# Performance work log

Hardware: AMD Instinct MI355X
Metric: run time of the kernel (lower is better)

The kernel has to match this reference:

```python
import jax, jax.numpy as jnp
import numpy as np

B, C, N = 32, 1024, 256   # N=256 is hard-coded by query/key Conv1d in_channels
DQ = 256 // 4             # 64
EPS = 1e-5                # BatchNorm eps


def setup_inputs() -> dict:
    key = jax.random.key(0)
    ks = jax.random.split(key, 16)
    def bn_params(k, ch):
        k1, k2, k3, k4 = jax.random.split(k, 4)
        return (jax.random.uniform(k1, (ch,), jnp.float32, 0.5, 1.5),   # gamma
                jax.random.normal(k2, (ch,), jnp.float32) * 0.1,        # beta
                jax.random.normal(k3, (ch,), jnp.float32) * 0.1,        # running mean
                jax.random.uniform(k4, (ch,), jnp.float32, 0.5, 1.5))   # running var
    bn1 = bn_params(ks[4], DQ)
    bn2 = bn_params(ks[5], DQ)
    bn3 = bn_params(ks[6], C)
    return {
        "x": jax.random.normal(ks[0], (B, C, N), jnp.float32),
        "Wq": jax.random.normal(ks[1], (DQ, N), jnp.float32) * (1.0 / np.sqrt(N)),
        "Wk": jax.random.normal(ks[2], (DQ, N), jnp.float32) * (1.0 / np.sqrt(N)),
        "Wv": jax.random.normal(ks[3], (C, C), jnp.float32) * (1.0 / np.sqrt(C)),
        "bn1_g": bn1[0], "bn1_b": bn1[1], "bn1_m": bn1[2], "bn1_v": bn1[3],
        "bn2_g": bn2[0], "bn2_b": bn2[1], "bn2_m": bn2[2], "bn2_v": bn2[3],
        "bn3_g": bn3[0], "bn3_b": bn3[1], "bn3_m": bn3[2], "bn3_v": bn3[3],
        "alpha": jnp.full((1,), 0.1, jnp.float32),  # torch init is 0; 0.1 keeps the branch active
    }


def _bn(y, g, b, m, v):
    # eval-mode BatchNorm1d over channel axis 1 of (B, ch, L)
    scale = g / jnp.sqrt(v + EPS)
    return (y - m[None, :, None]) * scale[None, :, None] + b[None, :, None]


def reference(x, Wq, Wk, Wv,
              bn1_g, bn1_b, bn1_m, bn1_v,
              bn2_g, bn2_b, bn2_m, bn2_v,
              bn3_g, bn3_b, bn3_m, bn3_v,
              alpha):
    x_hat = jnp.swapaxes(x, 1, 2)                                   # (B, N, C)
    q = jax.nn.relu(_bn(jnp.einsum('on,bnc->boc', Wq, x_hat), bn1_g, bn1_b, bn1_m, bn1_v))  # (B, DQ, C)
    k = jax.nn.relu(_bn(jnp.einsum('on,bnc->boc', Wk, x_hat), bn2_g, bn2_b, bn2_m, bn2_v))  # (B, DQ, C)
    sim = jnp.einsum('bkc,bkd->bcd', k, q)                          # (B, C, C) channel affinity
    aff = jax.nn.softmax(jnp.max(sim, axis=-1, keepdims=True) - sim, axis=-1)
    v = jax.nn.relu(_bn(jnp.einsum('oc,bcn->bon', Wv, x), bn3_g, bn3_b, bn3_m, bn3_v))      # (B, C, N)
    out = jnp.einsum('bcd,bdn->bcn', aff, v)                        # (B, C, N)
    return alpha * out + x
```

## Files before the change

kernel.cpp:

```cpp
#include <hip/hip_runtime.h>
#include <hip/hip_bf16.h>

#define B_  32
#define C_  1024
#define N_  256
#define DQ_ 64

typedef __bf16 bf16_t;
typedef __bf16 bf16x8 __attribute__((ext_vector_type(8)));
typedef float  f32x4  __attribute__((ext_vector_type(4)));

static __device__ __forceinline__ f32x4 mfma16(bf16x8 a, bf16x8 b, f32x4 c) {
  return __builtin_amdgcn_mfma_f32_16x16x32_bf16(a, b, c, 0, 0, 0);
}

static __device__ __forceinline__ bf16x8 ldcvt(const float* p) {
  const float4 a = *(const float4*)p;
  const float4 b = *(const float4*)(p + 4);
  bf16x8 r;
  r[0] = (bf16_t)a.x; r[1] = (bf16_t)a.y; r[2] = (bf16_t)a.z; r[3] = (bf16_t)a.w;
  r[4] = (bf16_t)b.x; r[5] = (bf16_t)b.y; r[6] = (bf16_t)b.z; r[7] = (bf16_t)b.w;
  return r;
}

#define WAIT_VMCNT(N) __builtin_amdgcn_s_waitcnt(0x0F70 | (N))

__global__ __launch_bounds__(256) void k_trans(const float* __restrict__ x,
                                               bf16_t* __restrict__ xT) {
  __shared__ bf16_t tile[32][34];
  const int b  = blockIdx.z;
  const int n0 = blockIdx.x * 32, c0 = blockIdx.y * 32;
  const int tx = threadIdx.x, ty = threadIdx.y;
  const float* xb = x + (size_t)b * C_ * N_;
  bf16_t*     xtb = xT + (size_t)b * N_ * C_;
#pragma unroll
  for (int i = 0; i < 4; ++i)
    tile[ty + i * 8][tx] = (bf16_t)xb[(size_t)(c0 + ty + i * 8) * N_ + (n0 + tx)];
  __syncthreads();
#pragma unroll
  for (int i = 0; i < 4; ++i)
    xtb[(size_t)(n0 + ty + i * 8) * C_ + (c0 + tx)] = tile[tx][ty + i * 8];
}

__global__ __launch_bounds__(256) void k_cvt(const float* __restrict__ Wv,
                                             const float* __restrict__ Wq,
                                             const float* __restrict__ Wk,
                                             bf16_t* __restrict__ Wvb,
                                             bf16_t* __restrict__ Wqkb) {
  const int gid = blockIdx.x * 256 + threadIdx.x;
  if (blockIdx.x < 512) {
    const int i = gid * 8;
    *(bf16x8*)(Wvb + i) = ldcvt(Wv + i);
  } else {
    const int g2 = (gid - 512 * 256) * 8;
    if (g2 < 16384) *(bf16x8*)(Wqkb + g2) = ldcvt(Wq + g2);
    else            *(bf16x8*)(Wqkb + g2) = ldcvt(Wk + (g2 - 16384));
  }
}

__global__ __launch_bounds__(256) void k_qk(const float* __restrict__ x,
                                            const bf16_t* __restrict__ Wqkb,
                                            const float* __restrict__ g1,
                                            const float* __restrict__ b1,
                                            const float* __restrict__ m1,
                                            const float* __restrict__ v1,
                                            const float* __restrict__ g2,
                                            const float* __restrict__ b2,
                                            const float* __restrict__ m2,
                                            const float* __restrict__ v2,
                                            bf16_t* __restrict__ qt,
                                            bf16_t* __restrict__ kt) {
  __shared__ __align__(16) bf16_t Ws[128 * 256];
  const int tid  = threadIdx.x;
  const int wave = tid >> 6;
  const int lane = tid & 63;
  const int quad = lane >> 4;
  const int l16  = lane & 15;
  const int b    = blockIdx.y;
  const int c16  = blockIdx.x * 64 + wave * 16;
  const float* xb = x + (size_t)b * C_ * N_;

#pragma unroll
  for (int t = 0; t < 16; ++t) {
    const int o = wave * 32 + t * 2 + (lane >> 5);
    const int s = lane & 31;
    const int g = (s - o) & 31;
    const bf16_t* src = Wqkb + (size_t)o * N_ + g * 8;
    __builtin_amdgcn_global_load_lds(
        (const __attribute__((address_space(1))) void*)src,
        (__attribute__((address_space(3))) void*)(Ws + (wave * 32 + t * 2) * N_ + lane * 8),
        16, 0, 0);
  }

  bf16x8 bx[8];
#pragma unroll
  for (int ks = 0; ks < 8; ++ks)
    bx[ks] = ldcvt(xb + (size_t)(c16 + l16) * N_ + ks * 32 + quad * 8);

  __syncthreads();

  f32x4 acc[8];
#pragma unroll
  for (int i = 0; i < 8; ++i) acc[i] = (f32x4){0.f, 0.f, 0.f, 0.f};

#pragma unroll
  for (int ks = 0; ks < 8; ++ks) {
    const int ch = ks * 4 + quad;
#pragma unroll
    for (int i = 0; i < 8; ++i) {
      const int orow = i * 16 + l16;
      const int s = (ch + orow) & 31;
      const bf16x8 aw = *(const bf16x8*)(Ws + (size_t)orow * N_ + s * 8);
      acc[i] = mfma16(aw, bx[ks], acc[i]);
    }
  }

#pragma unroll
  for (int i = 0; i < 8; ++i) {
    const bool isq = (i < 4);
    bf16_t* dst = isq ? qt : kt;
#pragma unroll
    for (int r = 0; r < 4; ++r) {
      const int o = (i & 3) * 16 + quad * 4 + r;
      const float sc = (isq ? g1[o] : g2[o]) * rsqrtf((isq ? v1[o] : v2[o]) + 1e-5f);
      const float mm = isq ? m1[o] : m2[o];
      const float bt = isq ? b1[o] : b2[o];
      const int c = c16 + l16;
      float y = (acc[i][r] - mm) * sc + bt;
      y = fmaxf(y, 0.f);
      dst[((size_t)b * C_ + c) * DQ_ + o] = (bf16_t)y;
    }
  }
}

static __device__ __forceinline__ void stage32(const bf16_t* grow0, size_t gstride,
                                               bf16_t* tile, int wave, int lane) {
#pragma unroll
  for (int t = 0; t < 4; ++t) {
    const int rb = wave * 32 + t * 8;
    const int r  = rb + (lane >> 3);
    const int g  = ((lane & 7) - r) & 7;
    const bf16_t* src = grow0 + (size_t)r * gstride + g * 8;
    __builtin_amdgcn_global_load_lds(
        (const __attribute__((address_space(1))) void*)src,
        (__attribute__((address_space(3))) void*)(tile + rb * 64), 16, 0, 0);
  }
}

__global__ __launch_bounds__(256, 2) void k_vgemm(const bf16_t* __restrict__ Wvb,
                                                  const bf16_t* __restrict__ xT,
                                                  const float* __restrict__ g,
                                                  const float* __restrict__ be,
                                                  const float* __restrict__ mu,
                                                  const float* __restrict__ va,
                                                  bf16_t* __restrict__ vT) {
  __shared__ __align__(16) bf16_t As[2][128 * 64];
  __shared__ __align__(16) bf16_t Bs[2][128 * 64];
  const int tid  = threadIdx.x;
  const int wave = tid >> 6;
  const int lane = tid & 63;
  const int quad = lane >> 4;
  const int l16  = lane & 15;
  const int o0 = blockIdx.x * 128;
  const int r0 = blockIdx.y * 128;
  const bf16_t* Ab = Wvb + (size_t)o0 * C_;
  const bf16_t* Bb = xT + (size_t)r0 * C_;
  const int wr = (wave >> 1) * 64, wc = (wave & 1) * 64;

  stage32(Ab, C_, (bf16_t*)As[0], wave, lane);
  stage32(Bb, C_, (bf16_t*)Bs[0], wave, lane);

  f32x4 acc[4][4];
#pragma unroll
  for (int i = 0; i < 4; ++i)
#pragma unroll
    for (int j = 0; j < 4; ++j) acc[i][j] = (f32x4){0.f, 0.f, 0.f, 0.f};

  for (int ks = 0; ks < 16; ++ks) {
    __syncthreads();
    const bf16_t* ca = As[ks & 1];
    const bf16_t* cb = Bs[ks & 1];
    if (ks < 15) {
      stage32(Ab + (ks + 1) * 64, C_, (bf16_t*)As[(ks + 1) & 1], wave, lane);
      stage32(Bb + (ks + 1) * 64, C_, (bf16_t*)Bs[(ks + 1) & 1], wave, lane);
    }
#pragma unroll
    for (int ksub = 0; ksub < 2; ++ksub) {
      bf16x8 a[4], bfr[4];
#pragma unroll
      for (int i = 0; i < 4; ++i) {
        const int r = wr + i * 16 + l16;
        const int s = ((ksub * 4 + quad) + r) & 7;
        a[i] = *(const bf16x8*)(ca + r * 64 + s * 8);
      }
#pragma unroll
      for (int j = 0; j < 4; ++j) {
        const int r = wc + j * 16 + l16;
        const int s = ((ksub * 4 + quad) + r) & 7;
        bfr[j] = *(const bf16x8*)(cb + r * 64 + s * 8);
      }
#pragma unroll
      for (int i = 0; i < 4; ++i)
#pragma unroll
        for (int j = 0; j < 4; ++j)
          acc[i][j] = mfma16(a[i], bfr[j], acc[i][j]);
    }
  }

#pragma unroll
  for (int i = 0; i < 4; ++i)
#pragma unroll
    for (int r = 0; r < 4; ++r) {
      const int o = o0 + wr + i * 16 + quad * 4 + r;
      const float sc = g[o] * rsqrtf(va[o] + 1e-5f);
      const float mm = mu[o], bt = be[o];
#pragma unroll
      for (int j = 0; j < 4; ++j) {
        const int rG = r0 + wc + j * 16 + l16;
        float y = (acc[i][j][r] - mm) * sc + bt;
        y = fmaxf(y, 0.f);
        vT[(size_t)rG * C_ + o] = (bf16_t)y;
      }
    }
}

static __device__ __forceinline__ int eaddr16(int c, int d) {
  const int ch = d >> 3;
  const int ph = (ch & ~7) | ((ch + c) & 7);
  return (c << 10) + (ph << 3) + (d & 7);
}

__global__ __launch_bounds__(256, 2) void k_fused(const bf16_t* __restrict__ qt,
                                                  const bf16_t* __restrict__ kt,
                                                  const bf16_t* __restrict__ vT,
                                                  const float* __restrict__ x,
                                                  const float* __restrict__ alphap,
                                                  float* __restrict__ out) {
  __shared__ __align__(16) bf16_t ebuf[16 * 1024];
  __shared__ __align__(16) bf16_t vs[2][4][64 * 32];
  __shared__ float redmin[4][16];
  __shared__ float redsum[4][16];
  __shared__ float rowmin[16];
  __shared__ float rowrinv[16];

  const int tid  = threadIdx.x;
  const int wave = tid >> 6;
  const int lane = tid & 63;
  const int quad = lane >> 4;
  const int l16  = lane & 15;
  const int id   = blockIdx.x;
  const int b    = ((id & 7) << 2) | (id >> 9);
  const int c0   = ((id >> 3) & 63) << 4;
  const int dbase = wave * 256;

  const bf16_t* ktb = kt + ((size_t)b * C_ + c0) * DQ_;
  const bf16_t* qb  = qt + (size_t)b * C_ * DQ_;
  bf16x8 am[2];
  am[0] = *(const bf16x8*)(ktb + (size_t)l16 * DQ_ + quad * 8);
  am[1] = *(const bf16x8*)(ktb + (size_t)l16 * DQ_ + 32 + quad * 8);
  f32x4 sim[16];
#pragma unroll
  for (int nt = 0; nt < 16; ++nt) {
    const bf16_t* qrow = qb + (size_t)(dbase + nt * 16 + l16) * DQ_ + quad * 8;
    const bf16x8 b0 = *(const bf16x8*)(qrow);
    const bf16x8 b1 = *(const bf16x8*)(qrow + 32);
    f32x4 acc = (f32x4){0.f, 0.f, 0.f, 0.f};
    acc = mfma16(am[0], b0, acc);
    acc = mfma16(am[1], b1, acc);
    sim[nt] = acc;
  }

  const bf16_t* vb = vT + ((size_t)b * N_ + wave * 64) * C_;
  bf16_t* myvs[2] = {(bf16_t*)vs[0][wave], (bf16_t*)vs[1][wave]};
#pragma unroll
  for (int t = 0; t < 4; ++t) {
    const int r = t * 16 + (lane >> 2);
    const int gg = ((lane & 3) - (r + (r >> 2))) & 3;
    const bf16_t* src = vb + (size_t)r * C_ + gg * 8;
    __builtin_amdgcn_global_load_lds(
        (const __attribute__((address_space(1))) void*)src,
        (__attribute__((address_space(3))) void*)(myvs[0] + t * 512 + lane * 8),
        16, 0, 0);
  }

  float pmin[4];
#pragma unroll
  for (int r = 0; r < 4; ++r) pmin[r] = sim[0][r];
#pragma unroll
  for (int nt = 1; nt < 16; ++nt)
#pragma unroll
    for (int r = 0; r < 4; ++r) pmin[r] = fminf(pmin[r], sim[nt][r]);
#pragma unroll
  for (int m = 1; m < 16; m <<= 1)
#pragma unroll
    for (int r = 0; r < 4; ++r) pmin[r] = fminf(pmin[r], __shfl_xor(pmin[r], m));
  if (l16 == 0)
#pragma unroll
    for (int r = 0; r < 4; ++r) redmin[wave][quad * 4 + r] = pmin[r];
  __syncthreads();
  if (tid < 16)
    rowmin[tid] = fminf(fminf(redmin[0][tid], redmin[1][tid]),
                        fminf(redmin[2][tid], redmin[3][tid]));
  __syncthreads();

  float mn[4], psum[4] = {0.f, 0.f, 0.f, 0.f};
#pragma unroll
  for (int r = 0; r < 4; ++r) mn[r] = rowmin[quad * 4 + r];
#pragma unroll
  for (int nt = 0; nt < 16; ++nt) {
    const int d = dbase + nt * 16 + l16;
#pragma unroll
    for (int r = 0; r < 4; ++r) {
      const int c = quad * 4 + r;
      const float e = __expf(mn[r] - sim[nt][r]);
      ebuf[eaddr16(c, d)] = (bf16_t)e;
      psum[r] += e;
    }
  }
#pragma unroll
  for (int m = 1; m < 16; m <<= 1)
#pragma unroll
    for (int r = 0; r < 4; ++r) psum[r] += __shfl_xor(psum[r], m);
  if (l16 == 0)
#pragma unroll
    for (int r = 0; r < 4; ++r) redsum[wave][quad * 4 + r] = psum[r];
  __syncthreads();
  if (tid < 16)
    rowrinv[tid] = 1.f / (redsum[0][tid] + redsum[1][tid] + redsum[2][tid] + redsum[3][tid]);
  __syncthreads();

  f32x4 oacc[4];
#pragma unroll
  for (int jn = 0; jn < 4; ++jn) oacc[jn] = (f32x4){0.f, 0.f, 0.f, 0.f};

  for (int ks = 0; ks < 32; ++ks) {
    const bf16_t* cur = myvs[ks & 1];
    if (ks < 31) {
      bf16_t* nxt = myvs[(ks + 1) & 1];
      const int koff = (ks + 1) * 32;
#pragma unroll
      for (int t = 0; t < 4; ++t) {
        const int r = t * 16 + (lane >> 2);
        const int gg = ((lane & 3) - (r + (r >> 2))) & 3;
        const bf16_t* src = vb + (size_t)r * C_ + koff + gg * 8;
        __builtin_amdgcn_global_load_lds(
            (const __attribute__((address_space(1))) void*)src,
            (__attribute__((address_space(3))) void*)(nxt + t * 512 + lane * 8),
            16, 0, 0);
      }
      WAIT_VMCNT(4);
    } else {
      WAIT_VMCNT(0);
    }
    const int gch = ks * 4 + quad;
    const int ph  = (gch & ~7) | ((gch + l16) & 7);
    const bf16x8 ae = *(const bf16x8*)(ebuf + ((size_t)l16 << 10) + ph * 8);
    bf16x8 bv[4];
#pragma unroll
    for (int jn = 0; jn < 4; ++jn) {
      const int rl = jn * 16 + l16;
      const int s = (quad + rl + (rl >> 2)) & 3;
      bv[jn] = *(const bf16x8*)(cur + rl * 32 + s * 8);
    }
#pragma unroll
    for (int jn = 0; jn < 4; ++jn)
      oacc[jn] = mfma16(ae, bv[jn], oacc[jn]);
  }

  const float alpha = alphap[0];
#pragma unroll
  for (int jn = 0; jn < 4; ++jn)
#pragma unroll
    for (int r = 0; r < 4; ++r) {
      const int c = c0 + quad * 4 + r;
      const int n = wave * 64 + jn * 16 + l16;
      const size_t idx = ((size_t)b * C_ + c) * N_ + n;
      out[idx] = alpha * (oacc[jn][r] * rowrinv[quad * 4 + r]) + x[idx];
    }
}

extern "C" void kernel_launch(void* const* d_in, const int* in_sizes, int n_in,
                              void* d_out, int out_size, void* d_ws, size_t ws_size,
                              hipStream_t stream) {
  const float* x    = (const float*)d_in[0];
  const float* Wq   = (const float*)d_in[1];
  const float* Wk   = (const float*)d_in[2];
  const float* Wv   = (const float*)d_in[3];
  const float* bn1g = (const float*)d_in[4];
  const float* bn1b = (const float*)d_in[5];
  const float* bn1m = (const float*)d_in[6];
  const float* bn1v = (const float*)d_in[7];
  const float* bn2g = (const float*)d_in[8];
  const float* bn2b = (const float*)d_in[9];
  const float* bn2m = (const float*)d_in[10];
  const float* bn2v = (const float*)d_in[11];
  const float* bn3g = (const float*)d_in[12];
  const float* bn3b = (const float*)d_in[13];
  const float* bn3m = (const float*)d_in[14];
  const float* bn3v = (const float*)d_in[15];
  const float* alph = (const float*)d_in[16];
  float* outp = (float*)d_out;

  char* ws = (char*)d_ws;
  bf16_t* qt   = (bf16_t*)(ws);
  bf16_t* kt   = (bf16_t*)(ws + (size_t)(4u << 20));
  bf16_t* vT   = (bf16_t*)(ws + (size_t)(8u << 20));
  bf16_t* xT   = (bf16_t*)(ws + (size_t)(24u << 20));
  bf16_t* Wvb  = (bf16_t*)(ws + (size_t)(40u << 20));
  bf16_t* Wqkb = (bf16_t*)(ws + (size_t)(42u << 20));

  k_trans<<<dim3(8, 32, 32), dim3(32, 8, 1), 0, stream>>>(x, xT);
  k_cvt<<<dim3(528), 256, 0, stream>>>(Wv, Wq, Wk, Wvb, Wqkb);
  k_qk<<<dim3(16, 32), 256, 0, stream>>>(x, Wqkb,
                                         bn1g, bn1b, bn1m, bn1v,
                                         bn2g, bn2b, bn2m, bn2v, qt, kt);
  k_vgemm<<<dim3(8, 64), 256, 0, stream>>>(Wvb, xT, bn3g, bn3b, bn3m, bn3v, vT);
  k_fused<<<dim3(2048), 256, 0, stream>>>(qt, kt, vT, x, alph, outp);
}
```

Before: 256.7 us.

## Restructure fused attention kernel: 32-row tiles, register softmax, split-K LDS reduction

Each block of the fused kernel now covers 32 channel rows instead of 16, which halves the grid. Each wave takes a 256-wide slice of the d dimension. The exp-softmax values stay in registers and are rearranged into MFMA A-fragments with cross-lane shuffles, so the LDS ebuf staging and the double-buffered async V loads are gone. Each wave then reads V directly from global memory over its own d slice and reduces partial outputs into a shared fp32 accumulator with LDS atomics before the final epilogue. The aim is to reuse V loads across 32 rows and remove LDS staging, at the cost of LDS atomic contention, unpipelined global loads, and a large shared buffer that may limit occupancy.

```diff
diff --git a/kernel.cpp b/kernel.cpp
--- a/kernel.cpp
+++ b/kernel.cpp
@@ -8,6 +8,7 @@
 
 typedef __bf16 bf16_t;
 typedef __bf16 bf16x8 __attribute__((ext_vector_type(8)));
+typedef __bf16 bf16x4 __attribute__((ext_vector_type(4)));
 typedef float  f32x4  __attribute__((ext_vector_type(4)));
 
 static __device__ __forceinline__ f32x4 mfma16(bf16x8 a, bf16x8 b, f32x4 c) {
@@ -22,8 +23,6 @@
   r[4] = (bf16_t)b.x; r[5] = (bf16_t)b.y; r[6] = (bf16_t)b.z; r[7] = (bf16_t)b.w;
   return r;
 }
-
-#define WAIT_VMCNT(N) __builtin_amdgcn_s_waitcnt(0x0F70 | (N))
 
 __global__ __launch_bounds__(256) void k_trans(const float* __restrict__ x,
                                                bf16_t* __restrict__ xT) {
@@ -224,24 +223,17 @@
     }
 }
 
-static __device__ __forceinline__ int eaddr16(int c, int d) {
-  const int ch = d >> 3;
-  const int ph = (ch & ~7) | ((ch + c) & 7);
-  return (c << 10) + (ph << 3) + (d & 7);
-}
-
 __global__ __launch_bounds__(256, 2) void k_fused(const bf16_t* __restrict__ qt,
                                                   const bf16_t* __restrict__ kt,
                                                   const bf16_t* __restrict__ vT,
                                                   const float* __restrict__ x,
                                                   const float* __restrict__ alphap,
                                                   float* __restrict__ out) {
-  __shared__ __align__(16) bf16_t ebuf[16 * 1024];
-  __shared__ __align__(16) bf16_t vs[2][4][64 * 32];
-  __shared__ float redmin[4][16];
-  __shared__ float redsum[4][16];
-  __shared__ float rowmin[16];
-  __shared__ float rowrinv[16];
+  __shared__ float outacc[32][257];
+  __shared__ float redmin[4][32];
+  __shared__ float redsum[4][32];
+  __shared__ float rowmin[32];
+  __shared__ float rowrinv[32];
 
   const int tid  = threadIdx.x;
   const int wave = tid >> 6;
@@ -249,134 +241,149 @@
   const int quad = lane >> 4;
   const int l16  = lane & 15;
   const int id   = blockIdx.x;
-  const int b    = ((id & 7) << 2) | (id >> 9);
-  const int c0   = ((id >> 3) & 63) << 4;
-  const int dbase = wave * 256;
-
+  const int b    = ((id & 7) << 2) | (id >> 8);
+  const int c0   = ((id >> 3) & 31) << 5;
+  const int d0   = wave * 256;
+
+  {
+    float* fl = &outacc[0][0];
+    for (int i = tid; i < 32 * 257; i += 256) fl[i] = 0.f;
+  }
+
+  const bf16_t* qb  = qt + (size_t)b * C_ * DQ_;
   const bf16_t* ktb = kt + ((size_t)b * C_ + c0) * DQ_;
-  const bf16_t* qb  = qt + (size_t)b * C_ * DQ_;
-  bf16x8 am[2];
-  am[0] = *(const bf16x8*)(ktb + (size_t)l16 * DQ_ + quad * 8);
-  am[1] = *(const bf16x8*)(ktb + (size_t)l16 * DQ_ + 32 + quad * 8);
-  f32x4 sim[16];
-#pragma unroll
-  for (int nt = 0; nt < 16; ++nt) {
-    const bf16_t* qrow = qb + (size_t)(dbase + nt * 16 + l16) * DQ_ + quad * 8;
-    const bf16x8 b0 = *(const bf16x8*)(qrow);
-    const bf16x8 b1 = *(const bf16x8*)(qrow + 32);
-    f32x4 acc = (f32x4){0.f, 0.f, 0.f, 0.f};
-    acc = mfma16(am[0], b0, acc);
-    acc = mfma16(am[1], b1, acc);
-    sim[nt] = acc;
-  }
-
-  const bf16_t* vb = vT + ((size_t)b * N_ + wave * 64) * C_;
-  bf16_t* myvs[2] = {(bf16_t*)vs[0][wave], (bf16_t*)vs[1][wave]};
-#pragma unroll
-  for (int t = 0; t < 4; ++t) {
-    const int r = t * 16 + (lane >> 2);
-    const int gg = ((lane & 3) - (r + (r >> 2))) & 3;
-    const bf16_t* src = vb + (size_t)r * C_ + gg * 8;
-    __builtin_amdgcn_global_load_lds(
-        (const __attribute__((address_space(1))) void*)src,
-        (__attribute__((address_space(3))) void*)(myvs[0] + t * 512 + lane * 8),
-        16, 0, 0);
-  }
-
-  float pmin[4];
-#pragma unroll
-  for (int r = 0; r < 4; ++r) pmin[r] = sim[0][r];
-#pragma unroll
-  for (int nt = 1; nt < 16; ++nt)
-#pragma unroll
-    for (int r = 0; r < 4; ++r) pmin[r] = fminf(pmin[r], sim[nt][r]);
-#pragma unroll
-  for (int m = 1; m < 16; m <<= 1)
-#pragma unroll
-    for (int r = 0; r < 4; ++r) pmin[r] = fminf(pmin[r], __shfl_xor(pmin[r], m));
-  if (l16 == 0)
-#pragma unroll
-    for (int r = 0; r < 4; ++r) redmin[wave][quad * 4 + r] = pmin[r];
-  __syncthreads();
-  if (tid < 16)
+  bf16x8 kf[2][2];
+#pragma unroll
+  for (int ci = 0; ci < 2; ++ci)
+#pragma unroll
+    for (int ks = 0; ks < 2; ++ks)
+      kf[ci][ks] = *(const bf16x8*)(ktb + (size_t)(ci * 16 + l16) * DQ_ + ks * 32 + quad * 8);
+
+  f32x4 sim[2][16];
+#pragma unroll
+  for (int ci = 0; ci < 2; ++ci)
+#pragma unroll
+    for (int dt = 0; dt < 16; ++dt) sim[ci][dt] = (f32x4){0.f, 0.f, 0.f, 0.f};
+
+#pragma unroll
+  for (int dt = 0; dt < 16; ++dt) {
+    const bf16_t* qrow = qb + (size_t)(d0 + dt * 16 + l16) * DQ_;
+    const bf16x8 q0 = *(const bf16x8*)(qrow + quad * 8);
+    const bf16x8 q1 = *(const bf16x8*)(qrow + 32 + quad * 8);
+#pragma unroll
+    for (int ci = 0; ci < 2; ++ci) {
+      sim[ci][dt] = mfma16(q0, kf[ci][0], sim[ci][dt]);
+      sim[ci][dt] = mfma16(q1, kf[ci][1], sim[ci][dt]);
+    }
+  }
+
+  float pmin[2];
+#pragma unroll
+  for (int ci = 0; ci < 2; ++ci) {
+    float m = sim[ci][0][0];
+#pragma unroll
+    for (int dt = 0; dt < 16; ++dt)
+#pragma unroll
+      for (int r = 0; r < 4; ++r) m = fminf(m, sim[ci][dt][r]);
+    m = fminf(m, __shfl_xor(m, 16));
+    m = fminf(m, __shfl_xor(m, 32));
+    pmin[ci] = m;
+  }
+  if (lane < 16) {
+    redmin[wave][l16]      = pmin[0];
+    redmin[wave][16 + l16] = pmin[1];
+  }
+  __syncthreads();
+  if (tid < 32)
     rowmin[tid] = fminf(fminf(redmin[0][tid], redmin[1][tid]),
                         fminf(redmin[2][tid], redmin[3][tid]));
   __syncthreads();
 
-  float mn[4], psum[4] = {0.f, 0.f, 0.f, 0.f};
-#pragma unroll
-  for (int r = 0; r < 4; ++r) mn[r] = rowmin[quad * 4 + r];
-#pragma unroll
-  for (int nt = 0; nt < 16; ++nt) {
-    const int d = dbase + nt * 16 + l16;
-#pragma unroll
-    for (int r = 0; r < 4; ++r) {
-      const int c = quad * 4 + r;
-      const float e = __expf(mn[r] - sim[nt][r]);
-      ebuf[eaddr16(c, d)] = (bf16_t)e;
-      psum[r] += e;
-    }
-  }
-#pragma unroll
-  for (int m = 1; m < 16; m <<= 1)
-#pragma unroll
-    for (int r = 0; r < 4; ++r) psum[r] += __shfl_xor(psum[r], m);
-  if (l16 == 0)
-#pragma unroll
-    for (int r = 0; r < 4; ++r) redsum[wave][quad * 4 + r] = psum[r];
-  __syncthreads();
-  if (tid < 16)
+  union U2 { bf16x4 v; uint2 u; };
+  U2 E[2][16];
+  float psum[2];
+#pragma unroll
+  for (int ci = 0; ci < 2; ++ci) {
+    const float mn = rowmin[ci * 16 + l16];
+    float s = 0.f;
+#pragma unroll
+    for (int dt = 0; dt < 16; ++dt) {
+      bf16x4 ev;
+#pragma unroll
+      for (int r = 0; r < 4; ++r) {
+        const float e = __expf(mn - sim[ci][dt][r]);
+        ev[r] = (bf16_t)e;
+        s += e;
+      }
+      E[ci][dt].v = ev;
+    }
+    s += __shfl_xor(s, 16);
+    s += __shfl_xor(s, 32);
+    psum[ci] = s;
+  }
+  if (lane < 16) {
+    redsum[wave][l16]      = psum[0];
+    redsum[wave][16 + l16] = psum[1];
+  }
+  __syncthreads();
+  if (tid < 32)
     rowrinv[tid] = 1.f / (redsum[0][tid] + redsum[1][tid] + redsum[2][tid] + redsum[3][tid]);
   __syncthreads();
 
-  f32x4 oacc[4];
-#pragma unroll
-  for (int jn = 0; jn < 4; ++jn) oacc[jn] = (f32x4){0.f, 0.f, 0.f, 0.f};
-
-  for (int ks = 0; ks < 32; ++ks) {
-    const bf16_t* cur = myvs[ks & 1];
-    if (ks < 31) {
-      bf16_t* nxt = myvs[(ks + 1) & 1];
-      const int koff = (ks + 1) * 32;
-#pragma unroll
-      for (int t = 0; t < 4; ++t) {
-        const int r = t * 16 + (lane >> 2);
-        const int gg = ((lane & 3) - (r + (r >> 2))) & 3;
-        const bf16_t* src = vb + (size_t)r * C_ + koff + gg * 8;
-        __builtin_amdgcn_global_load_lds(
-            (const __attribute__((address_space(1))) void*)src,
-            (__attribute__((address_space(3))) void*)(nxt + t * 512 + lane * 8),
-            16, 0, 0);
-      }
-      WAIT_VMCNT(4);
-    } else {
-      WAIT_VMCNT(0);
-    }
-    const int gch = ks * 4 + quad;
-    const int ph  = (gch & ~7) | ((gch + l16) & 7);
-    const bf16x8 ae = *(const bf16x8*)(ebuf + ((size_t)l16 << 10) + ph * 8);
-    bf16x8 bv[4];
-#pragma unroll
-    for (int jn = 0; jn < 4; ++jn) {
-      const int rl = jn * 16 + l16;
-      const int s = (quad + rl + (rl >> 2)) & 3;
-      bv[jn] = *(const bf16x8*)(cur + rl * 32 + s * 8);
-    }
-#pragma unroll
-    for (int jn = 0; jn < 4; ++jn)
-      oacc[jn] = mfma16(ae, bv[jn], oacc[jn]);
-  }
+  const int src0 = ((quad & 1) << 5) + l16;
+  const int src1 = src0 + 16;
+  const bool hiTile = (quad >> 1) & 1;
+  union U4 { bf16x8 v; uint4 u; };
+  U4 afrag[2][8];
+#pragma unroll
+  for (int ci = 0; ci < 2; ++ci)
+#pragma unroll
+    for (int p = 0; p < 8; ++p) {
+      uint2 e0 = E[ci][2 * p].u, e1 = E[ci][2 * p + 1].u;
+      const unsigned a0x = __shfl((int)e0.x, src0), a0y = __shfl((int)e0.y, src0);
+      const unsigned b0x = __shfl((int)e1.x, src0), b0y = __shfl((int)e1.y, src0);
+      const unsigned a1x = __shfl((int)e0.x, src1), a1y = __shfl((int)e0.y, src1);
+      const unsigned b1x = __shfl((int)e1.x, src1), b1y = __shfl((int)e1.y, src1);
+      U4 f;
+      f.u.x = hiTile ? b0x : a0x;
+      f.u.y = hiTile ? b0y : a0y;
+      f.u.z = hiTile ? b1x : a1x;
+      f.u.w = hiTile ? b1y : a1y;
+      afrag[ci][p] = f;
+    }
+
+  const bf16_t* vb = vT + (size_t)b * N_ * C_ + d0;
+#pragma unroll 2
+  for (int jn = 0; jn < 16; ++jn) {
+    const bf16_t* vrow = vb + (size_t)(jn * 16 + l16) * C_;
+    bf16x8 bfr[8];
+#pragma unroll
+    for (int p = 0; p < 8; ++p)
+      bfr[p] = *(const bf16x8*)(vrow + p * 32 + quad * 8);
+    f32x4 oacc[2];
+    oacc[0] = (f32x4){0.f, 0.f, 0.f, 0.f};
+    oacc[1] = (f32x4){0.f, 0.f, 0.f, 0.f};
+#pragma unroll
+    for (int p = 0; p < 8; ++p) {
+      oacc[0] = mfma16(afrag[0][p].v, bfr[p], oacc[0]);
+      oacc[1] = mfma16(afrag[1][p].v, bfr[p], oacc[1]);
+    }
+    const int n = jn * 16 + l16;
+#pragma unroll
+    for (int ci = 0; ci < 2; ++ci)
+#pragma unroll
+      for (int r = 0; r < 4; ++r)
+        atomicAdd(&outacc[ci * 16 + quad * 4 + r][n], oacc[ci][r]);
+  }
+  __syncthreads();
 
   const float alpha = alphap[0];
-#pragma unroll
-  for (int jn = 0; jn < 4; ++jn)
-#pragma unroll
-    for (int r = 0; r < 4; ++r) {
-      const int c = c0 + quad * 4 + r;
-      const int n = wave * 64 + jn * 16 + l16;
-      const size_t idx = ((size_t)b * C_ + c) * N_ + n;
-      out[idx] = alpha * (oacc[jn][r] * rowrinv[quad * 4 + r]) + x[idx];
-    }
+  const int n = tid;
+  const float* xrow = x + ((size_t)b * C_ + c0) * N_ + n;
+  float* orow = out + ((size_t)b * C_ + c0) * N_ + n;
+#pragma unroll
+  for (int c = 0; c < 32; ++c)
+    orow[c * N_] = alpha * (outacc[c][n] * rowrinv[c]) + xrow[c * N_];
 }
 
 extern "C" void kernel_launch(void* const* d_in, const int* in_sizes, int n_in,
@@ -415,5 +422,5 @@
                                          bn1g, bn1b, bn1m, bn1v,
                                          bn2g, bn2b, bn2m, bn2v, qt, kt);
   k_vgemm<<<dim3(8, 64), 256, 0, stream>>>(Wvb, xT, bn3g, bn3b, bn3m, bn3v, vT);
-  k_fused<<<dim3(2048), 256, 0, stream>>>(qt, kt, vT, x, alph, outp);
-}
+  k_fused<<<dim3(1024), 256, 0, stream>>>(qt, kt, vT, x, alph, outp);
+}
```

Result: slower. 349.5 us (+36.2%).
